# Kernel tuning notes

Hardware: AMD Instinct MI355X
Metric: run time of the kernel (lower is better)

## Reference

```python
import jax, jax.numpy as jnp
import numpy as np

T, D, H, OUT = 32768, 1024, 2048, 1024
E, K = 8, 4
EPS = 1e-5


def setup_inputs() -> dict:
    key = jax.random.key(0)
    ks = jax.random.split(key, 10)
    s = 0.02
    return {
        "x": jax.random.normal(ks[0], (T, D), jnp.float32),
        "ln_gamma": jnp.ones((D,), jnp.float32),
        "ln_beta": jnp.zeros((D,), jnp.float32),
        "router_w": jax.random.normal(ks[1], (D, E), jnp.float32) * s,
        "router_b": jnp.zeros((E,), jnp.float32),
        "w1": jax.random.normal(ks[2], (E, D, H), jnp.float32) * s,
        "b1": jnp.zeros((E, H), jnp.float32),
        "w2": jax.random.normal(ks[3], (E, H, OUT), jnp.float32) * s,
        "b2": jnp.zeros((E, OUT), jnp.float32),
    }


def _layernorm(x, gamma, beta):
    mu = jnp.mean(x, axis=-1, keepdims=True)
    var = jnp.mean(jnp.square(x - mu), axis=-1, keepdims=True)
    return (x - mu) * jax.lax.rsqrt(var + EPS) * gamma + beta


def reference(x, ln_gamma, ln_beta, router_w, router_b, w1, b1, w2, b2):
    # pre-LayerNorm
    xn = _layernorm(x, ln_gamma, ln_beta)                      # [T, D]
    # router + top-k gate, softmax over the selected k logits
    logits = xn @ router_w + router_b                          # [T, E]
    top_vals, top_idx = jax.lax.top_k(logits, K)               # [T, K]
    gate = jax.nn.softmax(top_vals, axis=-1)                   # [T, K]
    # scatter gate weights back to dense [T, E] (top_idx unique per row)
    w_full = jnp.sum(jax.nn.one_hot(top_idx, E, dtype=gate.dtype) * gate[..., None], axis=-2)
    # streaming per-expert dense FFN + weighted accumulation (matches source)
    y = jnp.zeros((x.shape[0], OUT), dtype=x.dtype)
    for e in range(E):
        h = jax.nn.gelu(xn @ w1[e] + b1[e], approximate=False)  # [T, H]
        y = y + (h @ w2[e] + b2[e]) * w_full[:, e:e + 1]
    return y
```

## Files before the change

### kernel.cpp

```cpp
#include <hip/hip_runtime.h>
#include <hip/hip_bf16.h>
#include <math.h>

typedef unsigned short u16;
typedef __attribute__((ext_vector_type(8))) short short8;
typedef __attribute__((ext_vector_type(4))) float f32x4;
typedef __attribute__((ext_vector_type(4))) unsigned short u16x4;

constexpr int T_   = 32768;
constexpr int D_   = 1024;
constexpr int H_   = 2048;
constexpr int OUT_ = 1024;
constexpr int E_   = 8;
constexpr int MAXTILES_ = 1040;

__device__ __forceinline__ u16 f2bf(float f) {
    unsigned u = __float_as_uint(f);
    u += 0x7FFFu + ((u >> 16) & 1u);
    return (u16)(u >> 16);
}

__device__ __forceinline__ void gload_lds16(const u16* g, u16* l) {
    __builtin_amdgcn_global_load_lds(
        (const __attribute__((address_space(1))) unsigned int*)g,
        (__attribute__((address_space(3))) unsigned int*)l, 16, 0, 0);
}

__device__ __forceinline__ float gelu_exact(float v) {
    return 0.5f * v * (1.0f + erff(v * 0.70710678118654752f));
}

__global__ __launch_bounds__(256) void ln_router_kernel(
    const float* __restrict__ x, const float* __restrict__ gamma,
    const float* __restrict__ beta, const float* __restrict__ rw,
    const float* __restrict__ rb, u16* __restrict__ xn,
    unsigned* __restrict__ topk_idx, float* __restrict__ topk_gate)
{
    __shared__ float xn_lds[4 * 1024];
    __shared__ float rwT[8 * 1024];
    __shared__ float plog[4 * 32 * 8];

    const int tid  = threadIdx.x;
    const int lane = tid & 63;
    const int wave = tid >> 6;
    const int row  = blockIdx.x * 4 + wave;
    const float* xr = x + (size_t)row * D_;

#pragma unroll
    for (int it = 0; it < 8; ++it) {
        const int f0 = it * 1024 + tid * 4;
        float4 v4 = *(const float4*)(rw + f0);
        const int d  = f0 >> 3;
        const int e0 = (tid & 1) * 4;
        rwT[(e0 + 0) * 1024 + d] = v4.x;
        rwT[(e0 + 1) * 1024 + d] = v4.y;
        rwT[(e0 + 2) * 1024 + d] = v4.z;
        rwT[(e0 + 3) * 1024 + d] = v4.w;
    }

    float v[16];
#pragma unroll
    for (int j = 0; j < 4; ++j) {
        float4 t = *(const float4*)(xr + (j * 64 + lane) * 4);
        v[j*4+0] = t.x; v[j*4+1] = t.y; v[j*4+2] = t.z; v[j*4+3] = t.w;
    }
    float s = 0.f, ss = 0.f;
#pragma unroll
    for (int i = 0; i < 16; ++i) { s += v[i]; ss += v[i] * v[i]; }
#pragma unroll
    for (int st = 32; st > 0; st >>= 1) { s += __shfl_xor(s, st); ss += __shfl_xor(ss, st); }
    const float mu   = s * (1.0f / 1024.0f);
    const float var  = ss * (1.0f / 1024.0f) - mu * mu;
    const float rstd = rsqrtf(var + 1e-5f);

#pragma unroll
    for (int j = 0; j < 4; ++j) {
        const int d0 = (j * 64 + lane) * 4;
        float4 g4 = *(const float4*)(gamma + d0);
        float4 b4 = *(const float4*)(beta + d0);
        f32x4 xnv;
        xnv[0] = (v[j*4+0] - mu) * rstd * g4.x + b4.x;
        xnv[1] = (v[j*4+1] - mu) * rstd * g4.y + b4.y;
        xnv[2] = (v[j*4+2] - mu) * rstd * g4.z + b4.z;
        xnv[3] = (v[j*4+3] - mu) * rstd * g4.w + b4.w;
        *(f32x4*)(xn_lds + wave * 1024 + d0) = xnv;
        u16x4 pk;
        pk.x = f2bf(xnv[0]); pk.y = f2bf(xnv[1]);
        pk.z = f2bf(xnv[2]); pk.w = f2bf(xnv[3]);
        *(u16x4*)(xn + (size_t)row * D_ + d0) = pk;
    }
    __syncthreads();

    const int e    = lane >> 3;
    const int dseg = lane & 7;
    float part[4] = {0.f, 0.f, 0.f, 0.f};
#pragma unroll
    for (int ii = 0; ii < 8; ++ii) {
        const int q = dseg + (wave * 8 + ii) * 8;
        f32x4 rw4 = *(const f32x4*)(rwT + e * 1024 + q * 4);
#pragma unroll
        for (int r = 0; r < 4; ++r) {
            f32x4 x4 = *(const f32x4*)(xn_lds + r * 1024 + q * 4);
            part[r] += x4[0]*rw4[0] + x4[1]*rw4[1] + x4[2]*rw4[2] + x4[3]*rw4[3];
        }
    }
#pragma unroll
    for (int r = 0; r < 4; ++r)
        plog[(r * 32 + wave * 8 + dseg) * 8 + e] = part[r];
    __syncthreads();

    const int rr = wave;
    const int ee = (lane >> 3) & 7;
    const int s8 = lane & 7;
    float val = plog[(rr * 32 + s8) * 8 + ee] + plog[(rr * 32 + s8 + 8) * 8 + ee]
              + plog[(rr * 32 + s8 + 16) * 8 + ee] + plog[(rr * 32 + s8 + 24) * 8 + ee];
    val += __shfl_xor(val, 1);
    val += __shfl_xor(val, 2);
    val += __shfl_xor(val, 4);
    val += rb[ee];

    float vv[8];
#pragma unroll
    for (int k = 0; k < 8; ++k) vv[k] = __shfl(val, k * 8);

    if (lane == 0) {
        unsigned used = 0, pack = 0;
        float tv[4];
#pragma unroll
        for (int k = 0; k < 4; ++k) {
            float best = -3.4e38f; int bi = 0;
#pragma unroll
            for (int q = 0; q < 8; ++q)
                if (!((used >> q) & 1) && vv[q] > best) { best = vv[q]; bi = q; }
            used |= 1u << bi; tv[k] = best; pack |= (unsigned)bi << (8 * k);
        }
        float ex[4], sum = 0.f;
#pragma unroll
        for (int k = 0; k < 4; ++k) { ex[k] = expf(tv[k] - tv[0]); sum += ex[k]; }
        const float inv = 1.0f / sum;
        topk_idx[row] = pack;
#pragma unroll
        for (int k = 0; k < 4; ++k) topk_gate[row * 4 + k] = ex[k] * inv;
    }
}

__global__ __launch_bounds__(256) void transpose_cvt_kernel(
    const float* __restrict__ w1, const float* __restrict__ w2,
    u16* __restrict__ w1t, u16* __restrict__ w2t)
{
    __shared__ float lds[32][33];
    int t = blockIdx.x;
    const float* src; u16* dst; int R, C, rt, ct;
    if (t < 16384) {
        int e = t >> 11, loc = t & 2047;
        rt = loc >> 6; ct = loc & 63;
        src = w1 + (size_t)e * D_ * H_; dst = w1t + (size_t)e * D_ * H_;
        R = D_; C = H_;
    } else {
        t -= 16384;
        int e = t >> 11, loc = t & 2047;
        rt = loc >> 5; ct = loc & 31;
        src = w2 + (size_t)e * H_ * OUT_; dst = w2t + (size_t)e * H_ * OUT_;
        R = H_; C = OUT_;
    }
    const int r  = threadIdx.x >> 3;
    const int c4 = (threadIdx.x & 7) * 4;
    float4 val = *(const float4*)(src + (size_t)(rt * 32 + r) * C + ct * 32 + c4);
    lds[r][c4+0] = val.x; lds[r][c4+1] = val.y; lds[r][c4+2] = val.z; lds[r][c4+3] = val.w;
    __syncthreads();
    const int cc = threadIdx.x >> 3;
    const int r4 = (threadIdx.x & 7) * 4;
    u16x4 o;
    o.x = f2bf(lds[r4+0][cc]); o.y = f2bf(lds[r4+1][cc]);
    o.z = f2bf(lds[r4+2][cc]); o.w = f2bf(lds[r4+3][cc]);
    *(u16x4*)(dst + (size_t)(ct * 32 + cc) * R + rt * 32 + r4) = o;
}

__global__ __launch_bounds__(256) void pair_build_kernel(
    const unsigned* __restrict__ topk_idx, const float* __restrict__ topk_gate,
    int* __restrict__ pair_tok, float* __restrict__ pair_gate, int* __restrict__ gcount)
{
    __shared__ int lcnt[8], lbase[8];
    const int tok = blockIdx.x * 256 + threadIdx.x;
    if (threadIdx.x < 8) lcnt[threadIdx.x] = 0;
    __syncthreads();
    const unsigned pk = topk_idx[tok];
    int e[4], off[4]; float g[4];
#pragma unroll
    for (int k = 0; k < 4; ++k) {
        e[k] = (pk >> (8 * k)) & 255;
        g[k] = topk_gate[tok * 4 + k];
        off[k] = atomicAdd(&lcnt[e[k]], 1);
    }
    __syncthreads();
    if (threadIdx.x < 8) lbase[threadIdx.x] = atomicAdd(&gcount[threadIdx.x], lcnt[threadIdx.x]);
    __syncthreads();
#pragma unroll
    for (int k = 0; k < 4; ++k) {
        int pos = lbase[e[k]] + off[k];
        pair_tok[e[k] * T_ + pos]  = tok;
        pair_gate[e[k] * T_ + pos] = g[k];
    }
}

__global__ void scan_kernel(const int* __restrict__ gcount, int* __restrict__ meta)
{
    const int t = threadIdx.x;
    if (t < 8) {
        int tiles_before = 0, rows_before = 0;
        for (int i = 0; i < t; ++i) {
            int c = gcount[i];
            int nt = (c + 127) >> 7;
            tiles_before += nt; rows_before += nt << 7;
        }
        int c  = gcount[t];
        int nt = (c + 127) >> 7;
        meta[1 + t] = rows_before;
        for (int i = 0; i < nt; ++i) meta[32 + tiles_before + i] = (t << 16) | i;
        if (t == 7) meta[0] = tiles_before + nt;
    }
}

__global__ __launch_bounds__(256) void gemm1_grouped(
    const u16* __restrict__ xn, const u16* __restrict__ w1t,
    const float* __restrict__ b1, const int* __restrict__ pair_tok,
    const int* __restrict__ gcount, const int* __restrict__ meta,
    u16* __restrict__ h)
{
    const int tile = blockIdx.y;
    if (tile >= meta[0]) return;
    const int dsc  = meta[32 + tile];
    const int e    = dsc >> 16;
    const int mloc = dsc & 0xffff;
    const int nt   = blockIdx.x;
    const int* ptok = pair_tok + e * T_;
    const u16* w1t_e = w1t + (size_t)e * D_ * H_;
    const float* b1_e = b1 + (size_t)e * H_;
    u16* hbase = h + (size_t)(meta[1 + e] + mloc * 128) * H_;

    __shared__ __align__(16) u16 As[128 * 32];
    __shared__ __align__(16) u16 Bs[128 * 32];

    const int tid  = threadIdx.x;
    const int lane = tid & 63;
    const int wave = tid >> 6;
    const int rs0 = tid >> 2;
    const int kg0 = (tid & 3) ^ ((rs0 >> 1) & 3);

    const int tokA0 = ptok[mloc * 128 + rs0];
    const int tokA1 = ptok[mloc * 128 + 64 + rs0];
    const u16* gA0 = xn + (size_t)tokA0 * D_ + kg0 * 8;
    const u16* gA1 = xn + (size_t)tokA1 * D_ + kg0 * 8;
    const u16* gB0 = w1t_e + (size_t)(nt * 128 + rs0) * D_ + kg0 * 8;
    const u16* gB1 = w1t_e + (size_t)(nt * 128 + 64 + rs0) * D_ + kg0 * 8;

    u16* AsW = As + wave * 512;
    u16* BsW = Bs + wave * 512;

    const int wm = (wave >> 1) * 64;
    const int wn = (wave & 1) * 64;
    const int fr = lane & 15;
    const int swz = (((lane >> 4) ^ ((fr >> 1) & 3))) * 8;

    f32x4 acc[4][4];
#pragma unroll
    for (int i = 0; i < 4; ++i)
#pragma unroll
        for (int j = 0; j < 4; ++j) acc[i][j] = (f32x4)0.0f;

    for (int kk = 0; kk < D_ / 32; ++kk) {
        gload_lds16(gA0, AsW);
        gload_lds16(gA1, AsW + 2048);
        gload_lds16(gB0, BsW);
        gload_lds16(gB1, BsW + 2048);
        gA0 += 32; gA1 += 32; gB0 += 32; gB1 += 32;
        __syncthreads();
        short8 a[4], b[4];
#pragma unroll
        for (int i = 0; i < 4; ++i) a[i] = *(const short8*)(As + (wm + i * 16 + fr) * 32 + swz);
#pragma unroll
        for (int i = 0; i < 4; ++i) b[i] = *(const short8*)(Bs + (wn + i * 16 + fr) * 32 + swz);
#pragma unroll
        for (int i = 0; i < 4; ++i)
#pragma unroll
            for (int j = 0; j < 4; ++j)
                acc[i][j] = __builtin_amdgcn_mfma_f32_16x16x32_bf16(a[i], b[j], acc[i][j], 0, 0, 0);
        __syncthreads();
    }

    const int cq = lane >> 4;
    const int cc = lane & 15;
#pragma unroll
    for (int j = 0; j < 4; ++j) {
        const int gcol = nt * 128 + wn + j * 16 + cc;
        const float bias = b1_e[gcol];
#pragma unroll
        for (int i = 0; i < 4; ++i) {
            const int lr0 = wm + i * 16 + cq * 4;
#pragma unroll
            for (int r = 0; r < 4; ++r) {
                float vv = gelu_exact(acc[i][j][r] + bias);
                hbase[(size_t)(lr0 + r) * H_ + gcol] = f2bf(vv);
            }
        }
    }
}

__global__ __launch_bounds__(256) void gemm2_grouped(
    const u16* __restrict__ h, const u16* __restrict__ w2t,
    const float* __restrict__ b2, const int* __restrict__ pair_tok,
    const float* __restrict__ pair_gate, const int* __restrict__ gcount,
    const int* __restrict__ meta, float* __restrict__ y)
{
    const int tile = blockIdx.y;
    if (tile >= meta[0]) return;
    const int dsc  = meta[32 + tile];
    const int e    = dsc >> 16;
    const int mloc = dsc & 0xffff;
    const int count = gcount[e];
    const int nt   = blockIdx.x;
    const int* ptok = pair_tok + e * T_;
    const float* pgate = pair_gate + e * T_;
    const u16* w2t_e = w2t + (size_t)e * OUT_ * H_;
    const float* b2_e = b2 + (size_t)e * OUT_;
    const u16* hbase = h + (size_t)(meta[1 + e] + mloc * 128) * H_;

    __shared__ __align__(16) u16 As[128 * 32];
    __shared__ __align__(16) u16 Bs[128 * 32];

    const int tid  = threadIdx.x;
    const int lane = tid & 63;
    const int wave = tid >> 6;
    const int rs0 = tid >> 2;
    const int kg0 = (tid & 3) ^ ((rs0 >> 1) & 3);

    const u16* gA0 = hbase + (size_t)rs0 * H_ + kg0 * 8;
    const u16* gA1 = hbase + (size_t)(64 + rs0) * H_ + kg0 * 8;
    const u16* gB0 = w2t_e + (size_t)(nt * 128 + rs0) * H_ + kg0 * 8;
    const u16* gB1 = w2t_e + (size_t)(nt * 128 + 64 + rs0) * H_ + kg0 * 8;

    u16* AsW = As + wave * 512;
    u16* BsW = Bs + wave * 512;

    const int wm = (wave >> 1) * 64;
    const int wn = (wave & 1) * 64;
    const int fr = lane & 15;
    const int swz = (((lane >> 4) ^ ((fr >> 1) & 3))) * 8;

    f32x4 acc[4][4];
#pragma unroll
    for (int i = 0; i < 4; ++i)
#pragma unroll
        for (int j = 0; j < 4; ++j) acc[i][j] = (f32x4)0.0f;

    for (int kk = 0; kk < H_ / 32; ++kk) {
        gload_lds16(gA0, AsW);
        gload_lds16(gA1, AsW + 2048);
        gload_lds16(gB0, BsW);
        gload_lds16(gB1, BsW + 2048);
        gA0 += 32; gA1 += 32; gB0 += 32; gB1 += 32;
        __syncthreads();
        short8 a[4], b[4];
#pragma unroll
        for (int i = 0; i < 4; ++i) a[i] = *(const short8*)(As + (wm + i * 16 + fr) * 32 + swz);
#pragma unroll
        for (int i = 0; i < 4; ++i) b[i] = *(const short8*)(Bs + (wn + i * 16 + fr) * 32 + swz);
#pragma unroll
        for (int i = 0; i < 4; ++i)
#pragma unroll
            for (int j = 0; j < 4; ++j)
                acc[i][j] = __builtin_amdgcn_mfma_f32_16x16x32_bf16(a[i], b[j], acc[i][j], 0, 0, 0);
        __syncthreads();
    }

    const int cq = lane >> 4;
    const int cc = lane & 15;
#pragma unroll
    for (int i = 0; i < 4; ++i) {
#pragma unroll
        for (int r = 0; r < 4; ++r) {
            const int lrow = wm + i * 16 + cq * 4 + r;
            if (mloc * 128 + lrow < count) {
                const int tok = ptok[mloc * 128 + lrow];
                const float g = pgate[mloc * 128 + lrow];
                float* yrow = y + (size_t)tok * OUT_;
#pragma unroll
                for (int j = 0; j < 4; ++j) {
                    const int gcol = nt * 128 + wn + j * 16 + cc;
                    atomicAdd(&yrow[gcol], g * (acc[i][j][r] + b2_e[gcol]));
                }
            }
        }
    }
}

__global__ __launch_bounds__(256) void gemm1_kernel(
    const u16* __restrict__ xn, const u16* __restrict__ w1t_e,
    const float* __restrict__ b1_e, const int* __restrict__ ptok,
    const int* __restrict__ pcount, u16* __restrict__ h)
{
    const int count = *pcount;
    const int mt = blockIdx.y;
    if (mt * 128 >= count) return;
    const int nt = blockIdx.x;
    __shared__ __align__(16) u16 As[128 * 32];
    __shared__ __align__(16) u16 Bs[128 * 32];
    const int tid  = threadIdx.x;
    const int lane = tid & 63;
    const int wave = tid >> 6;
    const int rs0 = tid >> 2;
    const int kg0 = (tid & 3) ^ ((rs0 >> 1) & 3);
    const int tokA0 = ptok[mt * 128 + rs0];
    const int tokA1 = ptok[mt * 128 + 64 + rs0];
    const u16* gA0 = xn + (size_t)tokA0 * D_ + kg0 * 8;
    const u16* gA1 = xn + (size_t)tokA1 * D_ + kg0 * 8;
    const u16* gB0 = w1t_e + (size_t)(nt * 128 + rs0) * D_ + kg0 * 8;
    const u16* gB1 = w1t_e + (size_t)(nt * 128 + 64 + rs0) * D_ + kg0 * 8;
    u16* AsW = As + wave * 512;
    u16* BsW = Bs + wave * 512;
    const int wm = (wave >> 1) * 64;
    const int wn = (wave & 1) * 64;
    const int fr = lane & 15;
    const int swz = (((lane >> 4) ^ ((fr >> 1) & 3))) * 8;
    f32x4 acc[4][4];
#pragma unroll
    for (int i = 0; i < 4; ++i)
#pragma unroll
        for (int j = 0; j < 4; ++j) acc[i][j] = (f32x4)0.0f;
    for (int kk = 0; kk < D_ / 32; ++kk) {
        gload_lds16(gA0, AsW); gload_lds16(gA1, AsW + 2048);
        gload_lds16(gB0, BsW); gload_lds16(gB1, BsW + 2048);
        gA0 += 32; gA1 += 32; gB0 += 32; gB1 += 32;
        __syncthreads();
        short8 a[4], b[4];
#pragma unroll
        for (int i = 0; i < 4; ++i) a[i] = *(const short8*)(As + (wm + i * 16 + fr) * 32 + swz);
#pragma unroll
        for (int i = 0; i < 4; ++i) b[i] = *(const short8*)(Bs + (wn + i * 16 + fr) * 32 + swz);
#pragma unroll
        for (int i = 0; i < 4; ++i)
#pragma unroll
            for (int j = 0; j < 4; ++j)
                acc[i][j] = __builtin_amdgcn_mfma_f32_16x16x32_bf16(a[i], b[j], acc[i][j], 0, 0, 0);
        __syncthreads();
    }
    const int cq = lane >> 4;
    const int cc = lane & 15;
#pragma unroll
    for (int j = 0; j < 4; ++j) {
        const int gcol = nt * 128 + wn + j * 16 + cc;
        const float bias = b1_e[gcol];
#pragma unroll
        for (int i = 0; i < 4; ++i) {
            const int grow0 = mt * 128 + wm + i * 16 + cq * 4;
#pragma unroll
            for (int r = 0; r < 4; ++r) {
                float vv = gelu_exact(acc[i][j][r] + bias);
                h[(size_t)(grow0 + r) * H_ + gcol] = f2bf(vv);
            }
        }
    }
}

__global__ __launch_bounds__(256) void gemm2_kernel(
    const u16* __restrict__ h, const u16* __restrict__ w2t_e,
    const float* __restrict__ b2_e, const int* __restrict__ ptok,
    const float* __restrict__ pgate, const int* __restrict__ pcount,
    float* __restrict__ y)
{
    const int count = *pcount;
    const int mt = blockIdx.y;
    if (mt * 128 >= count) return;
    const int nt = blockIdx.x;
    __shared__ __align__(16) u16 As[128 * 32];
    __shared__ __align__(16) u16 Bs[128 * 32];
    const int tid  = threadIdx.x;
    const int lane = tid & 63;
    const int wave = tid >> 6;
    const int rs0 = tid >> 2;
    const int kg0 = (tid & 3) ^ ((rs0 >> 1) & 3);
    const u16* gA0 = h + (size_t)(mt * 128 + rs0) * H_ + kg0 * 8;
    const u16* gA1 = h + (size_t)(mt * 128 + 64 + rs0) * H_ + kg0 * 8;
    const u16* gB0 = w2t_e + (size_t)(nt * 128 + rs0) * H_ + kg0 * 8;
    const u16* gB1 = w2t_e + (size_t)(nt * 128 + 64 + rs0) * H_ + kg0 * 8;
    u16* AsW = As + wave * 512;
    u16* BsW = Bs + wave * 512;
    const int wm = (wave >> 1) * 64;
    const int wn = (wave & 1) * 64;
    const int fr = lane & 15;
    const int swz = (((lane >> 4) ^ ((fr >> 1) & 3))) * 8;
    f32x4 acc[4][4];
#pragma unroll
    for (int i = 0; i < 4; ++i)
#pragma unroll
        for (int j = 0; j < 4; ++j) acc[i][j] = (f32x4)0.0f;
    for (int kk = 0; kk < H_ / 32; ++kk) {
        gload_lds16(gA0, AsW); gload_lds16(gA1, AsW + 2048);
        gload_lds16(gB0, BsW); gload_lds16(gB1, BsW + 2048);
        gA0 += 32; gA1 += 32; gB0 += 32; gB1 += 32;
        __syncthreads();
        short8 a[4], b[4];
#pragma unroll
        for (int i = 0; i < 4; ++i) a[i] = *(const short8*)(As + (wm + i * 16 + fr) * 32 + swz);
#pragma unroll
        for (int i = 0; i < 4; ++i) b[i] = *(const short8*)(Bs + (wn + i * 16 + fr) * 32 + swz);
#pragma unroll
        for (int i = 0; i < 4; ++i)
#pragma unroll
            for (int j = 0; j < 4; ++j)
                acc[i][j] = __builtin_amdgcn_mfma_f32_16x16x32_bf16(a[i], b[j], acc[i][j], 0, 0, 0);
        __syncthreads();
    }
    const int cq = lane >> 4;
    const int cc = lane & 15;
#pragma unroll
    for (int i = 0; i < 4; ++i) {
#pragma unroll
        for (int r = 0; r < 4; ++r) {
            const int irow = mt * 128 + wm + i * 16 + cq * 4 + r;
            if (irow < count) {
                const int tok = ptok[irow];
                const float g = pgate[irow];
                float* yrow = y + (size_t)tok * OUT_;
#pragma unroll
                for (int j = 0; j < 4; ++j) {
                    const int gcol = nt * 128 + wn + j * 16 + cc;
                    yrow[gcol] += g * (acc[i][j][r] + b2_e[gcol]);
                }
            }
        }
    }
}

extern "C" void kernel_launch(void* const* d_in, const int* in_sizes, int n_in,
                              void* d_out, int out_size, void* d_ws, size_t ws_size,
                              hipStream_t stream)
{
    const float* x     = (const float*)d_in[0];
    const float* gamma = (const float*)d_in[1];
    const float* beta  = (const float*)d_in[2];
    const float* rw    = (const float*)d_in[3];
    const float* rb    = (const float*)d_in[4];
    const float* w1    = (const float*)d_in[5];
    const float* b1    = (const float*)d_in[6];
    const float* w2    = (const float*)d_in[7];
    const float* b2    = (const float*)d_in[8];
    float* y = (float*)d_out;

    char* ws = (char*)d_ws;
    const size_t xn_off   = 0;
    const size_t w1t_off  = 67108864;
    const size_t w2t_off  = 100663296;
    const size_t ptok_off = 134217728;
    const size_t pgat_off = 135266304;
    const size_t tidx_off = 136314880;
    const size_t tgat_off = 136445952;
    const size_t meta_off = 136970240;
    const size_t gcnt_off = 136978432;
    const size_t h_off    = 137363456;
    const size_t h_grouped_bytes = (size_t)(131072 + E_ * 128) * H_ * 2;
    const size_t need_grouped = h_off + h_grouped_bytes;

    u16*      xn        = (u16*)(ws + xn_off);
    u16*      w1t       = (u16*)(ws + w1t_off);
    u16*      w2t       = (u16*)(ws + w2t_off);
    int*      pair_tok  = (int*)(ws + ptok_off);
    float*    pair_gate = (float*)(ws + pgat_off);
    unsigned* topk_idx  = (unsigned*)(ws + tidx_off);
    float*    topk_gate = (float*)(ws + tgat_off);
    int*      meta      = (int*)(ws + meta_off);
    int*      gcount    = (int*)(ws + gcnt_off);
    u16*      h         = (u16*)(ws + h_off);

    hipMemsetAsync(gcount, 0, 32, stream);
    hipMemsetAsync(pair_tok, 0, (size_t)E_ * T_ * 4, stream);
    hipMemsetAsync(d_out, 0, (size_t)T_ * OUT_ * 4, stream);

    ln_router_kernel<<<T_ / 4, 256, 0, stream>>>(x, gamma, beta, rw, rb, xn, topk_idx, topk_gate);
    transpose_cvt_kernel<<<32768, 256, 0, stream>>>(w1, w2, w1t, w2t);
    pair_build_kernel<<<T_ / 256, 256, 0, stream>>>(topk_idx, topk_gate, pair_tok, pair_gate, gcount);

    if (ws_size >= need_grouped) {
        scan_kernel<<<1, 64, 0, stream>>>(gcount, meta);
        gemm1_grouped<<<dim3(H_ / 128, MAXTILES_), 256, 0, stream>>>(
            xn, w1t, b1, pair_tok, gcount, meta, h);
        gemm2_grouped<<<dim3(OUT_ / 128, MAXTILES_), 256, 0, stream>>>(
            h, w2t, b2, pair_tok, pair_gate, gcount, meta, y);
    } else {
        for (int e = 0; e < E_; ++e) {
            gemm1_kernel<<<dim3(H_ / 128, T_ / 128), 256, 0, stream>>>(
                xn, w1t + (size_t)e * H_ * D_, b1 + (size_t)e * H_,
                pair_tok + (size_t)e * T_, gcount + e, h);
            gemm2_kernel<<<dim3(OUT_ / 128, T_ / 128), 256, 0, stream>>>(
                h, w2t + (size_t)e * OUT_ * H_, b2 + (size_t)e * OUT_,
                pair_tok + (size_t)e * T_, pair_gate + (size_t)e * T_, gcount + e, y);
        }
    }
}
```

Baseline: 2.451 ms.

## Chunk grouped expert GEMMs to fit the intermediate buffer in available workspace

The grouped GEMM1/GEMM2 pair now runs in chunks of tiles sized to the available workspace, instead of needing room for the whole intermediate activation. Each chunk writes into a small reused slice of the buffer, and GEMM2 consumes it before the next chunk starts. When the full buffer did not fit, this lets the single grouped launch per GEMM replace the per-expert fallback of 16 mostly empty launches. The cost is more launches, and the two GEMMs serialise at every chunk boundary.

Result: no change. 2.458 ms (+0.3%).

```diff
diff --git a/kernel.cpp b/kernel.cpp
--- a/kernel.cpp
+++ b/kernel.cpp
@@ -225,9 +225,9 @@
     const u16* __restrict__ xn, const u16* __restrict__ w1t,
     const float* __restrict__ b1, const int* __restrict__ pair_tok,
     const int* __restrict__ gcount, const int* __restrict__ meta,
-    u16* __restrict__ h)
-{
-    const int tile = blockIdx.y;
+    u16* __restrict__ h, int chunk_base)
+{
+    const int tile = chunk_base + blockIdx.y;
     if (tile >= meta[0]) return;
     const int dsc  = meta[32 + tile];
     const int e    = dsc >> 16;
@@ -236,7 +236,7 @@
     const int* ptok = pair_tok + e * T_;
     const u16* w1t_e = w1t + (size_t)e * D_ * H_;
     const float* b1_e = b1 + (size_t)e * H_;
-    u16* hbase = h + (size_t)(meta[1 + e] + mloc * 128) * H_;
+    u16* hbase = h + (size_t)blockIdx.y * 128 * H_;
 
     __shared__ __align__(16) u16 As[128 * 32];
     __shared__ __align__(16) u16 Bs[128 * 32];
@@ -310,9 +310,9 @@
     const u16* __restrict__ h, const u16* __restrict__ w2t,
     const float* __restrict__ b2, const int* __restrict__ pair_tok,
     const float* __restrict__ pair_gate, const int* __restrict__ gcount,
-    const int* __restrict__ meta, float* __restrict__ y)
-{
-    const int tile = blockIdx.y;
+    const int* __restrict__ meta, float* __restrict__ y, int chunk_base)
+{
+    const int tile = chunk_base + blockIdx.y;
     if (tile >= meta[0]) return;
     const int dsc  = meta[32 + tile];
     const int e    = dsc >> 16;
@@ -323,7 +323,7 @@
     const float* pgate = pair_gate + e * T_;
     const u16* w2t_e = w2t + (size_t)e * OUT_ * H_;
     const float* b2_e = b2 + (size_t)e * OUT_;
-    const u16* hbase = h + (size_t)(meta[1 + e] + mloc * 128) * H_;
+    const u16* hbase = h + (size_t)blockIdx.y * 128 * H_;
 
     __shared__ __align__(16) u16 As[128 * 32];
     __shared__ __align__(16) u16 Bs[128 * 32];
@@ -558,8 +558,6 @@
     const size_t meta_off = 136970240;
     const size_t gcnt_off = 136978432;
     const size_t h_off    = 137363456;
-    const size_t h_grouped_bytes = (size_t)(131072 + E_ * 128) * H_ * 2;
-    const size_t need_grouped = h_off + h_grouped_bytes;
 
     u16*      xn        = (u16*)(ws + xn_off);
     u16*      w1t       = (u16*)(ws + w1t_off);
@@ -580,12 +578,20 @@
     transpose_cvt_kernel<<<32768, 256, 0, stream>>>(w1, w2, w1t, w2t);
     pair_build_kernel<<<T_ / 256, 256, 0, stream>>>(topk_idx, topk_gate, pair_tok, pair_gate, gcount);
 
-    if (ws_size >= need_grouped) {
+    const size_t tile_bytes = (size_t)128 * H_ * 2;
+    size_t avail = (ws_size > h_off) ? (ws_size - h_off) : 0;
+    int CT = (int)(avail / tile_bytes);
+    if (CT > MAXTILES_) CT = MAXTILES_;
+
+    if (CT >= 64) {
         scan_kernel<<<1, 64, 0, stream>>>(gcount, meta);
-        gemm1_grouped<<<dim3(H_ / 128, MAXTILES_), 256, 0, stream>>>(
-            xn, w1t, b1, pair_tok, gcount, meta, h);
-        gemm2_grouped<<<dim3(OUT_ / 128, MAXTILES_), 256, 0, stream>>>(
-            h, w2t, b2, pair_tok, pair_gate, gcount, meta, y);
+        for (int base = 0; base < MAXTILES_; base += CT) {
+            const int tiles = (MAXTILES_ - base < CT) ? (MAXTILES_ - base) : CT;
+            gemm1_grouped<<<dim3(H_ / 128, tiles), 256, 0, stream>>>(
+                xn, w1t, b1, pair_tok, gcount, meta, h, base);
+            gemm2_grouped<<<dim3(OUT_ / 128, tiles), 256, 0, stream>>>(
+                h, w2t, b2, pair_tok, pair_gate, gcount, meta, y, base);
+        }
     } else {
         for (int e = 0; e < E_; ++e) {
             gemm1_kernel<<<dim3(H_ / 128, T_ / 128), 256, 0, stream>>>(
```
